# Performance work log

Hardware: AMD Instinct MI355X
Metric: run time of the kernel (lower is better)

Reference implementation:

```python
import jax, jax.numpy as jnp
import numpy as np

N_NODES = 50000
N_EDGES = 800000
HEADS = 4
IN_CH = 64
# hidden_dims=[32,64] reversed -> per-head out channels [64, 32]; concat=True
C1, C2 = 64, 32          # layer per-head channels
OUT_CH = 64              # conv_recon per-head channels, concat=False
NEG_SLOPE = 0.2


def gat_conv(x, edge_src, edge_dst, W, a_src, a_dst, b, concat):
    """PyG GATConv (v1) forward, eval mode (no dropout).
    x: [N, F_in]; W: [F_in, H*C]; a_src/a_dst: [H, C]; b: [H*C] or [C].
    edge (j -> i): messages flow edge_src -> edge_dst; softmax grouped by dst.
    """
    N = x.shape[0]
    H, C = a_src.shape
    h = (x @ W).reshape(N, H, C)                    # [N, H, C]
    al_s = jnp.einsum('nhc,hc->nh', h, a_src)       # [N, H]
    al_d = jnp.einsum('nhc,hc->nh', h, a_dst)       # [N, H]
    e = al_s[edge_src] + al_d[edge_dst]             # [E, H]
    e = jax.nn.leaky_relu(e, negative_slope=NEG_SLOPE)
    # segment softmax over incoming edges of each dst node
    m = jax.ops.segment_max(e, edge_dst, num_segments=N)          # [N, H]
    ex = jnp.exp(e - m[edge_dst])                                  # [E, H]
    s = jax.ops.segment_sum(ex, edge_dst, num_segments=N)         # [N, H]
    alpha = ex / (s[edge_dst] + 1e-16)                             # [E, H]
    msg = h[edge_src] * alpha[:, :, None]                          # [E, H, C]
    out = jax.ops.segment_sum(msg, edge_dst, num_segments=N)      # [N, H, C]
    out = out.reshape(N, H * C) if concat else out.mean(axis=1)
    return out + b


def setup_inputs() -> dict:
    key = jax.random.key(0)
    ks = jax.random.split(key, 16)
    sc = 0.1
    inp = {
        'x': jax.random.normal(ks[0], (N_NODES, IN_CH), jnp.float32),
        'edge_index': jax.random.randint(ks[1], (2, N_EDGES), 0, N_NODES, jnp.int64),
        # layer 1: in 64 -> 4 heads x 64, concat -> 256
        'W1': jax.random.normal(ks[2], (IN_CH, HEADS * C1), jnp.float32) * sc,
        'a1_src': jax.random.normal(ks[3], (HEADS, C1), jnp.float32) * sc,
        'a1_dst': jax.random.normal(ks[4], (HEADS, C1), jnp.float32) * sc,
        'b1': jnp.zeros((HEADS * C1,), jnp.float32),
        # layer 2: in 256 -> 4 heads x 32, concat -> 128
        'W2': jax.random.normal(ks[5], (HEADS * C1, HEADS * C2), jnp.float32) * sc,
        'a2_src': jax.random.normal(ks[6], (HEADS, C2), jnp.float32) * sc,
        'a2_dst': jax.random.normal(ks[7], (HEADS, C2), jnp.float32) * sc,
        'b2': jnp.zeros((HEADS * C2,), jnp.float32),
        # conv_recon: in 128 -> 4 heads x 64, concat=False (mean) -> 64
        'W3': jax.random.normal(ks[8], (HEADS * C2, HEADS * OUT_CH), jnp.float32) * sc,
        'a3_src': jax.random.normal(ks[9], (HEADS, OUT_CH), jnp.float32) * sc,
        'a3_dst': jax.random.normal(ks[10], (HEADS, OUT_CH), jnp.float32) * sc,
        'b3': jnp.zeros((OUT_CH,), jnp.float32),
    }
    return inp


def reference(x, edge_index, W1, a1_src, a1_dst, b1, W2, a2_src, a2_dst, b2,
              W3, a3_src, a3_dst, b3):
    src, dst = edge_index[0], edge_index[1]
    # used_DSBN=False -> no norm/ReLU between layers (matches torch forward)
    h = gat_conv(x, src, dst, W1, a1_src, a1_dst, b1, concat=True)
    h = gat_conv(h, src, dst, W2, a2_src, a2_dst, b2, concat=True)
    recon = gat_conv(h, src, dst, W3, a3_src, a3_dst, b3, concat=False)
    return recon
```

## Files before the change

### kernel.cpp

```cpp
#include <hip/hip_runtime.h>
#include <hip/hip_bf16.h>

#define HEADS 4

typedef __attribute__((ext_vector_type(4))) float f32x4;
typedef __attribute__((ext_vector_type(8))) short s16x8;

__device__ __forceinline__ float u2f(unsigned short u) {
    return __uint_as_float(((unsigned)u) << 16);
}
__device__ __forceinline__ unsigned short rne(float v) {
    unsigned b = __float_as_uint(v);
    return (unsigned short)((b + 0x7FFF + ((b >> 16) & 1)) >> 16);
}
__device__ __forceinline__ float ld1(const float* p) { return *p; }
__device__ __forceinline__ float ld1(const __hip_bfloat16* p) {
    return u2f(*reinterpret_cast<const unsigned short*>(p));
}
__device__ __forceinline__ float2 ld2(const float* p) { return *reinterpret_cast<const float2*>(p); }
__device__ __forceinline__ float2 ld2(const __hip_bfloat16* p) {
    ushort2 u = *reinterpret_cast<const ushort2*>(p);
    return make_float2(u2f(u.x), u2f(u.y));
}
__device__ __forceinline__ float4 ld4(const float* p) { return *reinterpret_cast<const float4*>(p); }
__device__ __forceinline__ float4 ld4(const __hip_bfloat16* p) {
    ushort4 u = *reinterpret_cast<const ushort4*>(p);
    return make_float4(u2f(u.x), u2f(u.y), u2f(u.z), u2f(u.w));
}
__device__ __forceinline__ void st1(float* p, float v) { *p = v; }
__device__ __forceinline__ void st1(__hip_bfloat16* p, float v) {
    *reinterpret_cast<unsigned short*>(p) = rne(v);
}
__device__ __forceinline__ void st2(float* p, float a, float b) {
    *reinterpret_cast<float2*>(p) = make_float2(a, b);
}
__device__ __forceinline__ void st2(__hip_bfloat16* p, float a, float b) {
    *reinterpret_cast<ushort2*>(p) = make_ushort2(rne(a), rne(b));
}
__device__ __forceinline__ void st4(float* p, float4 v) { *reinterpret_cast<float4*>(p) = v; }
__device__ __forceinline__ void st4(__hip_bfloat16* p, float4 v) {
    *reinterpret_cast<ushort4*>(p) = make_ushort4(rne(v.x), rne(v.y), rne(v.z), rne(v.w));
}

__device__ __forceinline__ int detect64(const int* __restrict__ e) {
    return ((e[1] | e[3] | e[5] | e[7]) == 0) ? 1 : 0;
}
__device__ __forceinline__ int edge_elem(const int* e, size_t idx, int is64) {
    return is64 ? e[2 * idx] : e[idx];
}

__global__ void deg_kernel(const int* __restrict__ eidx, int* __restrict__ deg, int E, int N) {
    int e = blockIdx.x * blockDim.x + threadIdx.x;
    if (e < E) {
        int is64 = detect64(eidx);
        int d = edge_elem(eidx, (size_t)E + e, is64);
        if ((unsigned)d < (unsigned)N) atomicAdd(&deg[d], 1);
    }
}

__global__ void reduce_kernel(const int* __restrict__ deg, int* __restrict__ bsum, int n) {
    __shared__ int sdata[256];
    int base = blockIdx.x * 1024;
    int t = threadIdx.x;
    int v = 0;
#pragma unroll
    for (int j = 0; j < 4; ++j) {
        int i = base + t + j * 256;
        if (i < n) v += deg[i];
    }
    sdata[t] = v;
    __syncthreads();
    for (int off = 128; off > 0; off >>= 1) {
        if (t < off) sdata[t] += sdata[t + off];
        __syncthreads();
    }
    if (t == 0) bsum[blockIdx.x] = sdata[0];
}

__global__ void scan_bsum_kernel(const int* __restrict__ bsum, int* __restrict__ boff,
                                 int nb, int* __restrict__ totalp) {
    int lane = threadIdx.x;
    int carry = 0;
    for (int base = 0; base < nb; base += 64) {
        int i = base + lane;
        int v = (i < nb) ? bsum[i] : 0;
        int inc = v;
        for (int off = 1; off < 64; off <<= 1) {
            int tt = __shfl_up(inc, off);
            if (lane >= off) inc += tt;
        }
        if (i < nb) boff[i] = carry + inc - v;
        carry += __shfl(inc, 63);
    }
    if (lane == 0) *totalp = carry;
}

__global__ void block_scan_kernel(const int* __restrict__ deg, const int* __restrict__ boff,
                                  int* __restrict__ rowptr, int* __restrict__ cursor, int n) {
    __shared__ int wsum[4];
    int base = blockIdx.x * 1024;
    int t = threadIdx.x;
    int lane = t & 63, w = t >> 6;
    int v[4];
    int lsum = 0;
#pragma unroll
    for (int j = 0; j < 4; ++j) {
        int i = base + t * 4 + j;
        v[j] = (i < n) ? deg[i] : 0;
        lsum += v[j];
    }
    int inc = lsum;
    for (int off = 1; off < 64; off <<= 1) {
        int tt = __shfl_up(inc, off);
        if (lane >= off) inc += tt;
    }
    if (lane == 63) wsum[w] = inc;
    __syncthreads();
    int woff = 0;
    for (int i = 0; i < w; ++i) woff += wsum[i];
    int ex = boff[blockIdx.x] + woff + inc - lsum;
#pragma unroll
    for (int j = 0; j < 4; ++j) {
        int i = base + t * 4 + j;
        if (i < n) { rowptr[i] = ex; cursor[i] = ex; }
        ex += v[j];
    }
}

__global__ void scatter_kernel(const int* __restrict__ eidx, int* __restrict__ cursor,
                               int* __restrict__ csr_src, int E, int N) {
    int e = blockIdx.x * blockDim.x + threadIdx.x;
    if (e < E) {
        int is64 = detect64(eidx);
        int s = edge_elem(eidx, (size_t)e, is64);
        int d = edge_elem(eidx, (size_t)E + e, is64);
        if ((unsigned)d < (unsigned)N && (unsigned)s < (unsigned)N) {
            int pos = atomicAdd(&cursor[d], 1);
            csr_src[pos] = s;
        }
    }
}

__global__ void prep0_kernel(const float* __restrict__ W1, const float* __restrict__ W2,
                             const float* __restrict__ W3, const float* __restrict__ b1,
                             const float* __restrict__ a1s, const float* __restrict__ a1d,
                             const float* __restrict__ a3s, const float* __restrict__ a3d,
                             __hip_bfloat16* __restrict__ Bt3, __hip_bfloat16* __restrict__ BtF,
                             float* __restrict__ bias12,
                             float* __restrict__ ps1, float* __restrict__ pd1,
                             float* __restrict__ ps3, float* __restrict__ pd3) {
    int b = blockIdx.x, t = threadIdx.x;
    if (b < 128) {
        int idx = b * 256 + t;
        int c = idx >> 9, r = idx & 511;
        int h = r >> 7, kk = r & 127;
        st1(&Bt3[idx], W3[(size_t)kk * 256 + h * 64 + c] * 0.25f);
        return;
    }
    b -= 128;
    if (b < 128) {
        int idx = b * 256 + t;
        int m = idx >> 8, k = idx & 255;
        int h = k >> 6, kin = k & 63;
        float acc = 0.f;
        for (int c = 0; c < 64; ++c)
            acc += W1[(size_t)kin * 256 + h * 64 + c] * W2[(size_t)(h * 64 + c) * 128 + m];
        st1(&BtF[idx], acc);
        return;
    }
    b -= 128;
    if (b < 1) {
        if (t < 128) {
            float acc = 0.f;
            for (int j = 0; j < 256; ++j) acc += b1[j] * W2[(size_t)j * 128 + t];
            bias12[t] = acc;
        }
        return;
    }
    b -= 1;
    if (b < 1) {
        int h = t >> 6, k = t & 63;
        float ss = 0.f, sd = 0.f;
        for (int c = 0; c < 64; ++c) {
            float w = W1[(size_t)k * 256 + h * 64 + c];
            ss += w * a1s[h * 64 + c];
            sd += w * a1d[h * 64 + c];
        }
        ps1[t] = ss;
        pd1[t] = sd;
        return;
    }
    b -= 1;
    if (b < 2) {
        int idx = b * 256 + t;
        int h = idx >> 7, k = idx & 127;
        float ss = 0.f, sd = 0.f;
        for (int c = 0; c < 64; ++c) {
            float w = W3[(size_t)k * 256 + h * 64 + c];
            ss += w * a3s[h * 64 + c];
            sd += w * a3d[h * 64 + c];
        }
        ps3[idx] = ss;
        pd3[idx] = sd;
        return;
    }
}

__global__ void xconv_alx_kernel(const float* __restrict__ x, const float* __restrict__ ps1,
                                 const float* __restrict__ pd1, __hip_bfloat16* __restrict__ xb,
                                 float* __restrict__ als, float* __restrict__ ald, int n8) {
    int i = blockIdx.x * blockDim.x + threadIdx.x;
    if (i >= n8) return;
    int r = i >> 3, sub = i & 7;
    int cbase = sub * 8;
    float4 a = *reinterpret_cast<const float4*>(&x[(size_t)i * 8]);
    float4 c = *reinterpret_cast<const float4*>(&x[(size_t)i * 8 + 4]);
    st4(&xb[(size_t)i * 8], a);
    st4(&xb[(size_t)i * 8 + 4], c);
    float ss[4], sd[4];
#pragma unroll
    for (int h = 0; h < 4; ++h) {
        float4 s0 = *reinterpret_cast<const float4*>(&ps1[h * 64 + cbase]);
        float4 s1 = *reinterpret_cast<const float4*>(&ps1[h * 64 + cbase + 4]);
        float4 d0 = *reinterpret_cast<const float4*>(&pd1[h * 64 + cbase]);
        float4 d1 = *reinterpret_cast<const float4*>(&pd1[h * 64 + cbase + 4]);
        ss[h] = a.x * s0.x + a.y * s0.y + a.z * s0.z + a.w * s0.w
              + c.x * s1.x + c.y * s1.y + c.z * s1.z + c.w * s1.w;
        sd[h] = a.x * d0.x + a.y * d0.y + a.z * d0.z + a.w * d0.w
              + c.x * d1.x + c.y * d1.y + c.z * d1.z + c.w * d1.w;
    }
#pragma unroll
    for (int off = 1; off < 8; off <<= 1) {
#pragma unroll
        for (int h = 0; h < 4; ++h) {
            ss[h] += __shfl_xor(ss[h], off);
            sd[h] += __shfl_xor(sd[h], off);
        }
    }
    if (sub == 0) {
        *reinterpret_cast<float4*>(&als[(size_t)r * 4]) = make_float4(ss[0], ss[1], ss[2], ss[3]);
        *reinterpret_cast<float4*>(&ald[(size_t)r * 4]) = make_float4(sd[0], sd[1], sd[2], sd[3]);
    }
}

template <int C, typename T>
__global__ void al_kernel(const T* __restrict__ h,
                          const float* __restrict__ a_src, const float* __restrict__ a_dst,
                          float* __restrict__ al_s, float* __restrict__ al_d, int N) {
    int idx = blockIdx.x * blockDim.x + threadIdx.x;
    if (idx >= N * HEADS) return;
    int n = idx >> 2, hd = idx & 3;
    const T* row = h + (size_t)n * HEADS * C + hd * C;
    float ss = 0.f, sd = 0.f;
#pragma unroll
    for (int c = 0; c < C; c += 4) {
        float4 v = ld4(&row[c]);
        float4 as = *reinterpret_cast<const float4*>(&a_src[hd * C + c]);
        float4 ad = *reinterpret_cast<const float4*>(&a_dst[hd * C + c]);
        ss += v.x * as.x + v.y * as.y + v.z * as.z + v.w * as.w;
        sd += v.x * ad.x + v.y * ad.y + v.z * ad.z + v.w * ad.w;
    }
    al_s[idx] = ss;
    al_d[idx] = sd;
}

template <int K, typename TIN, typename TOUT>
__global__ void gather_pre_kernel(const TIN* __restrict__ x, const float* __restrict__ als,
                                  const float* __restrict__ ald, const int* __restrict__ rowptr,
                                  const int* __restrict__ csr, TOUT* __restrict__ agg, int N) {
    constexpr int V = K / 64;
    int wave = (blockIdx.x * blockDim.x + threadIdx.x) >> 6;
    int lane = threadIdx.x & 63;
    if (wave >= N) return;
    int h4 = lane & 3, e4 = lane >> 2;
    float aldv = ald[wave * 4 + h4];
    float s0 = 0.f, s1 = 0.f, s2 = 0.f, s3 = 0.f;
    float acc[4][V] = {};
    int beg = rowptr[wave], end = rowptr[wave + 1];
    for (int kc = beg; kc < end; kc += 16) {
        int cnt = end - kc;
        if (cnt > 16) cnt = 16;
        int j = kc + e4;
        int src = csr[(j < end) ? j : beg];
        float e = als[src * 4 + h4] + aldv;
        e = fmaxf(e, 0.2f * e);
        float myw = __expf(e);
        if (cnt == 16) {
            int sj[16];
#pragma unroll
            for (int jj = 0; jj < 16; ++jj) sj[jj] = __shfl(src, jj * 4);
            if (V == 1) {
                float pv[16];
#pragma unroll
                for (int jj = 0; jj < 16; ++jj) pv[jj] = ld1(&x[(size_t)sj[jj] * K + lane]);
#pragma unroll
                for (int jj = 0; jj < 16; ++jj) {
                    float w0 = __shfl(myw, jj * 4 + 0), w1 = __shfl(myw, jj * 4 + 1);
                    float w2 = __shfl(myw, jj * 4 + 2), w3 = __shfl(myw, jj * 4 + 3);
                    s0 += w0; s1 += w1; s2 += w2; s3 += w3;
                    acc[0][0] += w0 * pv[jj]; acc[1][0] += w1 * pv[jj];
                    acc[2][0] += w2 * pv[jj]; acc[3][0] += w3 * pv[jj];
                }
            } else {
                float2 pv[16];
#pragma unroll
                for (int jj = 0; jj < 16; ++jj) pv[jj] = ld2(&x[(size_t)sj[jj] * K + lane * 2]);
#pragma unroll
                for (int jj = 0; jj < 16; ++jj) {
                    float w0 = __shfl(myw, jj * 4 + 0), w1 = __shfl(myw, jj * 4 + 1);
                    float w2 = __shfl(myw, jj * 4 + 2), w3 = __shfl(myw, jj * 4 + 3);
                    s0 += w0; s1 += w1; s2 += w2; s3 += w3;
                    acc[0][0] += w0 * pv[jj].x; acc[0][1] += w0 * pv[jj].y;
                    acc[1][0] += w1 * pv[jj].x; acc[1][1] += w1 * pv[jj].y;
                    acc[2][0] += w2 * pv[jj].x; acc[2][1] += w2 * pv[jj].y;
                    acc[3][0] += w3 * pv[jj].x; acc[3][1] += w3 * pv[jj].y;
                }
            }
        } else {
            for (int jj = 0; jj < cnt; ++jj) {
                int sjj = __shfl(src, jj * 4);
                float w0 = __shfl(myw, jj * 4 + 0), w1 = __shfl(myw, jj * 4 + 1);
                float w2 = __shfl(myw, jj * 4 + 2), w3 = __shfl(myw, jj * 4 + 3);
                s0 += w0; s1 += w1; s2 += w2; s3 += w3;
                if (V == 1) {
                    float v = ld1(&x[(size_t)sjj * K + lane]);
                    acc[0][0] += w0 * v; acc[1][0] += w1 * v;
                    acc[2][0] += w2 * v; acc[3][0] += w3 * v;
                } else {
                    float2 v = ld2(&x[(size_t)sjj * K + lane * 2]);
                    acc[0][0] += w0 * v.x; acc[0][1] += w0 * v.y;
                    acc[1][0] += w1 * v.x; acc[1][1] += w1 * v.y;
                    acc[2][0] += w2 * v.x; acc[2][1] += w2 * v.y;
                    acc[3][0] += w3 * v.x; acc[3][1] += w3 * v.y;
                }
            }
        }
    }
    float inv[4] = {1.f / (s0 + 1e-16f), 1.f / (s1 + 1e-16f),
                    1.f / (s2 + 1e-16f), 1.f / (s3 + 1e-16f)};
    size_t o = (size_t)wave * 4 * K;
#pragma unroll
    for (int h = 0; h < 4; ++h) {
        if (V == 1) {
            st1(&agg[o + h * K + lane], acc[h][0] * inv[h]);
        } else {
            st2(&agg[o + h * K + lane * 2], acc[h][0] * inv[h], acc[h][1] * inv[h]);
        }
    }
}

template <typename TIN, typename TOUT>
__global__ void gather_post32_alx_kernel(
    const TIN* __restrict__ h2, const float* __restrict__ als,
    const float* __restrict__ ald, const int* __restrict__ rowptr,
    const int* __restrict__ csr, const float* __restrict__ bias,
    const float* __restrict__ ps3, const float* __restrict__ pd3,
    TOUT* __restrict__ outp,
    float* __restrict__ als3, float* __restrict__ ald3, int N) {
    int wave = (blockIdx.x * blockDim.x + threadIdx.x) >> 6;
    int lane = threadIdx.x & 63;
    if (wave >= N) return;
    int h4 = lane & 3, e4 = lane >> 2;
    int hh = lane >> 4, l16 = lane & 15;
    float aldv = ald[wave * 4 + h4];
    float s = 0.f, a0 = 0.f, a1 = 0.f;
    int beg = rowptr[wave], end = rowptr[wave + 1];
    for (int kc = beg; kc < end; kc += 16) {
        int cnt = end - kc;
        if (cnt > 16) cnt = 16;
        int j = kc + e4;
        int src = csr[(j < end) ? j : beg];
        float e = als[src * 4 + h4] + aldv;
        e = fmaxf(e, 0.2f * e);
        float myw = __expf(e);
        if (cnt == 16) {
            int sj[16];
#pragma unroll
            for (int jj = 0; jj < 16; ++jj) sj[jj] = __shfl(src, jj * 4);
            float2 pv[16];
#pragma unroll
            for (int jj = 0; jj < 16; ++jj)
                pv[jj] = ld2(&h2[(size_t)sj[jj] * 128 + hh * 32 + l16 * 2]);
#pragma unroll
            for (int jj = 0; jj < 16; ++jj) {
                float w = __shfl(myw, jj * 4 + hh);
                s += w;
                a0 += w * pv[jj].x;
                a1 += w * pv[jj].y;
            }
        } else {
            for (int jj = 0; jj < cnt; ++jj) {
                int sjj = __shfl(src, jj * 4);
                float w = __shfl(myw, jj * 4 + hh);
                s += w;
                float2 v = ld2(&h2[(size_t)sjj * 128 + hh * 32 + l16 * 2]);
                a0 += w * v.x;
                a1 += w * v.y;
            }
        }
    }
    float inv = 1.f / (s + 1e-16f);
    int c = hh * 32 + l16 * 2;
    float v0 = a0 * inv + bias[c];
    float v1 = a1 * inv + bias[c + 1];
    st2(&outp[(size_t)wave * 128 + c], v0, v1);

    float sArr[4], dArr[4];
#pragma unroll
    for (int h = 0; h < 4; ++h) {
        float2 vs = *reinterpret_cast<const float2*>(&ps3[h * 128 + c]);
        float2 vd = *reinterpret_cast<const float2*>(&pd3[h * 128 + c]);
        sArr[h] = v0 * vs.x + v1 * vs.y;
        dArr[h] = v0 * vd.x + v1 * vd.y;
    }
#pragma unroll
    for (int off = 1; off < 64; off <<= 1) {
#pragma unroll
        for (int h = 0; h < 4; ++h) {
            sArr[h] += __shfl_xor(sArr[h], off);
            dArr[h] += __shfl_xor(dArr[h], off);
        }
    }
    if (lane < 4) {
        float os = (lane == 0) ? sArr[0] : (lane == 1) ? sArr[1] : (lane == 2) ? sArr[2] : sArr[3];
        float od = (lane == 0) ? dArr[0] : (lane == 1) ? dArr[1] : (lane == 2) ? dArr[2] : dArr[3];
        als3[wave * 4 + lane] = os;
        ald3[wave * 4 + lane] = od;
    }
}

template <typename TOUT>
__global__ __launch_bounds__(256) void mfma_gemm_kernel(
    const __hip_bfloat16* __restrict__ A, int lda, int aSel,
    const __hip_bfloat16* __restrict__ Bt,
    TOUT* __restrict__ O, int ldo,
    const float* __restrict__ bias, int N, int K) {
    __shared__ __hip_bfloat16 As[128][40];
    __shared__ __hip_bfloat16 Bs[64][40];
    int col0 = blockIdx.x * 64;
    int row0 = blockIdx.y * 128;
    int aOff = aSel ? col0 : 0;
    int tid = threadIdx.x;
    int wv = tid >> 6, lane = tid & 63;
    int g = lane >> 4, l16 = lane & 15;
    f32x4 acc[2][4] = {};

    for (int k0 = 0; k0 < K; k0 += 32) {
#pragma unroll
        for (int i = 0; i < 2; ++i) {
            int idx = tid + i * 256;
            int r = idx >> 2, h4 = idx & 3;
            int gr = row0 + r;
            uint4 v = make_uint4(0, 0, 0, 0);
            if (gr < N) v = *reinterpret_cast<const uint4*>(&A[(size_t)gr * lda + aOff + k0 + h4 * 8]);
            *reinterpret_cast<uint4*>(&As[r][h4 * 8]) = v;
        }
        {
            int r = tid >> 2, h4 = tid & 3;
            uint4 v = *reinterpret_cast<const uint4*>(&Bt[(size_t)(col0 + r) * K + k0 + h4 * 8]);
            *reinterpret_cast<uint4*>(&Bs[r][h4 * 8]) = v;
        }
        __syncthreads();
        s16x8 af[2], bf[4];
#pragma unroll
        for (int m = 0; m < 2; ++m)
            af[m] = *reinterpret_cast<const s16x8*>(&As[wv * 32 + m * 16 + l16][g * 8]);
#pragma unroll
        for (int n = 0; n < 4; ++n)
            bf[n] = *reinterpret_cast<const s16x8*>(&Bs[n * 16 + l16][g * 8]);
#pragma unroll
        for (int m = 0; m < 2; ++m)
#pragma unroll
            for (int n = 0; n < 4; ++n)
                acc[m][n] = __builtin_amdgcn_mfma_f32_16x16x32_bf16(af[m], bf[n], acc[m][n], 0, 0, 0);
        __syncthreads();
    }
#pragma unroll
    for (int m = 0; m < 2; ++m) {
#pragma unroll
        for (int rr = 0; rr < 4; ++rr) {
            int row = row0 + wv * 32 + m * 16 + g * 4 + rr;
            if (row < N) {
#pragma unroll
                for (int n = 0; n < 4; ++n) {
                    int col = col0 + n * 16 + l16;
                    float v = acc[m][n][rr];
                    if (bias) v += bias[col];
                    st1(&O[(size_t)row * ldo + col], v);
                }
            }
        }
    }
}

extern "C" void kernel_launch(void* const* d_in, const int* in_sizes, int n_in,
                              void* d_out, int out_size, void* d_ws, size_t ws_size,
                              hipStream_t stream) {
    const float* x      = (const float*)d_in[0];
    const int*   eidx   = (const int*)d_in[1];
    const float* W1     = (const float*)d_in[2];
    const float* a1_src = (const float*)d_in[3];
    const float* a1_dst = (const float*)d_in[4];
    const float* b1     = (const float*)d_in[5];
    const float* W2     = (const float*)d_in[6];
    const float* a2_src = (const float*)d_in[7];
    const float* a2_dst = (const float*)d_in[8];
    const float* b2     = (const float*)d_in[9];
    const float* W3     = (const float*)d_in[10];
    const float* a3_src = (const float*)d_in[11];
    const float* a3_dst = (const float*)d_in[12];
    const float* b3     = (const float*)d_in[13];
    float* out = (float*)d_out;

    const int N = in_sizes[0] / 64;
    const int E = in_sizes[1] / 2;
    const int NB = (N + 1023) / 1024;

    int* rowptr = (int*)d_ws;
    int* deg    = rowptr + (N + 1);
    int* cursor = deg + N;
    int* csr    = cursor + N;
    int* bsum   = csr + E;
    int* boff   = bsum + NB;
    uintptr_t pa = (uintptr_t)(boff + NB);
    pa = (pa + 255) & ~(uintptr_t)255;
    float* als  = (float*)pa;
    float* ald  = als + (size_t)N * 4;
    float* als3 = ald + (size_t)N * 4;
    float* ald3 = als3 + (size_t)N * 4;
    float* ps1  = ald3 + (size_t)N * 4;
    float* pd1  = ps1 + 256;
    float* ps3  = pd1 + 256;
    float* pd3  = ps3 + 512;
    float* bias12 = pd3 + 512;
    __hip_bfloat16* Bt3 = (__hip_bfloat16*)(bias12 + 128);
    __hip_bfloat16* BtF = Bt3 + 64 * 512;
    uintptr_t pf = (uintptr_t)(BtF + 128 * 256);
    pf = (pf + 255) & ~(uintptr_t)255;
    float* F    = (float*)pf;

    __hip_bfloat16* xb    = (__hip_bfloat16*)F;
    __hip_bfloat16* agg1b = (__hip_bfloat16*)(F + (size_t)N * 32);
    __hip_bfloat16* h2b   = (__hip_bfloat16*)(F + (size_t)N * 160);
    __hip_bfloat16* out2b = (__hip_bfloat16*)(F + (size_t)N * 224);
    __hip_bfloat16* agg3  = (__hip_bfloat16*)(F + (size_t)N * 288);

    hipMemsetAsync(deg, 0, (size_t)N * sizeof(int), stream);
    deg_kernel<<<(E + 255) / 256, 256, 0, stream>>>(eidx, deg, E, N);
    reduce_kernel<<<NB, 256, 0, stream>>>(deg, bsum, N);
    scan_bsum_kernel<<<1, 64, 0, stream>>>(bsum, boff, NB, rowptr + N);
    block_scan_kernel<<<NB, 256, 0, stream>>>(deg, boff, rowptr, cursor, N);
    scatter_kernel<<<(E + 255) / 256, 256, 0, stream>>>(eidx, cursor, csr, E, N);

    prep0_kernel<<<128 + 128 + 1 + 1 + 2, 256, 0, stream>>>(
        W1, W2, W3, b1, a1_src, a1_dst, a3_src, a3_dst,
        Bt3, BtF, bias12, ps1, pd1, ps3, pd3);
    const int n8 = N * 8;
    xconv_alx_kernel<<<(n8 + 255) / 256, 256, 0, stream>>>(x, ps1, pd1, xb, als, ald, n8);

    const int alBlocks  = (N * HEADS + 255) / 256;
    const int aggBlocks = (N + 3) / 4;
    const int rowB128   = (N + 127) / 128;

    gather_pre_kernel<64, __hip_bfloat16, __hip_bfloat16><<<aggBlocks, 256, 0, stream>>>(
        xb, als, ald, rowptr, csr, agg1b, N);
    mfma_gemm_kernel<__hip_bfloat16><<<dim3(2, rowB128), 256, 0, stream>>>(
        agg1b, 256, 0, BtF, h2b, 128, bias12, N, 256);

    al_kernel<32, __hip_bfloat16><<<alBlocks, 256, 0, stream>>>(h2b, a2_src, a2_dst, als, ald, N);
    gather_post32_alx_kernel<__hip_bfloat16, __hip_bfloat16><<<aggBlocks, 256, 0, stream>>>(
        h2b, als, ald, rowptr, csr, b2, ps3, pd3, out2b, als3, ald3, N);

    gather_pre_kernel<128, __hip_bfloat16, __hip_bfloat16><<<aggBlocks, 256, 0, stream>>>(
        out2b, als3, ald3, rowptr, csr, agg3, N);
    mfma_gemm_kernel<float><<<dim3(1, rowB128), 256, 0, stream>>>(
        agg3, 512, 0, Bt3, out, 64, b3, N, 512);
}
```

Measured before the change: 338.7 us.

## Fuse layer-2 attention logits into GEMM epilogue and vectorize gather loads

Removes the separate al_kernel by computing per-head source and destination attention logits inside the MFMA GEMM epilogue, using lane shuffles over the 16-column groups. It also restructures gather_pre_kernel so each lane loads 4 contiguous features from one edge, with several edges processed in parallel per wave. Partial sums are then combined by an xor-shuffle reduction before the store. This trades wider, fewer memory transactions and one fewer launch for extra shuffle-reduction work and more accumulator registers.

```diff
diff --git a/kernel.cpp b/kernel.cpp
--- a/kernel.cpp
+++ b/kernel.cpp
@@ -243,39 +243,21 @@
     }
 }
 
-template <int C, typename T>
-__global__ void al_kernel(const T* __restrict__ h,
-                          const float* __restrict__ a_src, const float* __restrict__ a_dst,
-                          float* __restrict__ al_s, float* __restrict__ al_d, int N) {
-    int idx = blockIdx.x * blockDim.x + threadIdx.x;
-    if (idx >= N * HEADS) return;
-    int n = idx >> 2, hd = idx & 3;
-    const T* row = h + (size_t)n * HEADS * C + hd * C;
-    float ss = 0.f, sd = 0.f;
-#pragma unroll
-    for (int c = 0; c < C; c += 4) {
-        float4 v = ld4(&row[c]);
-        float4 as = *reinterpret_cast<const float4*>(&a_src[hd * C + c]);
-        float4 ad = *reinterpret_cast<const float4*>(&a_dst[hd * C + c]);
-        ss += v.x * as.x + v.y * as.y + v.z * as.z + v.w * as.w;
-        sd += v.x * ad.x + v.y * ad.y + v.z * ad.z + v.w * ad.w;
-    }
-    al_s[idx] = ss;
-    al_d[idx] = sd;
-}
-
 template <int K, typename TIN, typename TOUT>
 __global__ void gather_pre_kernel(const TIN* __restrict__ x, const float* __restrict__ als,
                                   const float* __restrict__ ald, const int* __restrict__ rowptr,
                                   const int* __restrict__ csr, TOUT* __restrict__ agg, int N) {
-    constexpr int V = K / 64;
+    constexpr int G = K / 4;
+    constexpr int EPI = 64 / G;
     int wave = (blockIdx.x * blockDim.x + threadIdx.x) >> 6;
     int lane = threadIdx.x & 63;
     if (wave >= N) return;
     int h4 = lane & 3, e4 = lane >> 2;
+    int slot = lane / G;
+    int cb = (lane & (G - 1)) * 4;
     float aldv = ald[wave * 4 + h4];
-    float s0 = 0.f, s1 = 0.f, s2 = 0.f, s3 = 0.f;
-    float acc[4][V] = {};
+    float s[4] = {};
+    float acc[4][4] = {};
     int beg = rowptr[wave], end = rowptr[wave + 1];
     for (int kc = beg; kc < end; kc += 16) {
         int cnt = end - kc;
@@ -284,67 +266,69 @@
         int src = csr[(j < end) ? j : beg];
         float e = als[src * 4 + h4] + aldv;
         e = fmaxf(e, 0.2f * e);
-        float myw = __expf(e);
+        float myw = (e4 < cnt) ? __expf(e) : 0.f;
         if (cnt == 16) {
-            int sj[16];
-#pragma unroll
-            for (int jj = 0; jj < 16; ++jj) sj[jj] = __shfl(src, jj * 4);
-            if (V == 1) {
-                float pv[16];
-#pragma unroll
-                for (int jj = 0; jj < 16; ++jj) pv[jj] = ld1(&x[(size_t)sj[jj] * K + lane]);
-#pragma unroll
-                for (int jj = 0; jj < 16; ++jj) {
-                    float w0 = __shfl(myw, jj * 4 + 0), w1 = __shfl(myw, jj * 4 + 1);
-                    float w2 = __shfl(myw, jj * 4 + 2), w3 = __shfl(myw, jj * 4 + 3);
-                    s0 += w0; s1 += w1; s2 += w2; s3 += w3;
-                    acc[0][0] += w0 * pv[jj]; acc[1][0] += w1 * pv[jj];
-                    acc[2][0] += w2 * pv[jj]; acc[3][0] += w3 * pv[jj];
-                }
-            } else {
-                float2 pv[16];
-#pragma unroll
-                for (int jj = 0; jj < 16; ++jj) pv[jj] = ld2(&x[(size_t)sj[jj] * K + lane * 2]);
-#pragma unroll
-                for (int jj = 0; jj < 16; ++jj) {
-                    float w0 = __shfl(myw, jj * 4 + 0), w1 = __shfl(myw, jj * 4 + 1);
-                    float w2 = __shfl(myw, jj * 4 + 2), w3 = __shfl(myw, jj * 4 + 3);
-                    s0 += w0; s1 += w1; s2 += w2; s3 += w3;
-                    acc[0][0] += w0 * pv[jj].x; acc[0][1] += w0 * pv[jj].y;
-                    acc[1][0] += w1 * pv[jj].x; acc[1][1] += w1 * pv[jj].y;
-                    acc[2][0] += w2 * pv[jj].x; acc[2][1] += w2 * pv[jj].y;
-                    acc[3][0] += w3 * pv[jj].x; acc[3][1] += w3 * pv[jj].y;
-                }
+            constexpr int IT = 16 / EPI;
+            int esrc[IT];
+#pragma unroll
+            for (int i = 0; i < IT; ++i) esrc[i] = __shfl(src, (i * EPI + slot) * 4);
+            float4 pv[IT];
+#pragma unroll
+            for (int i = 0; i < IT; ++i) pv[i] = ld4(&x[(size_t)esrc[i] * K + cb]);
+#pragma unroll
+            for (int i = 0; i < IT; ++i) {
+                int base = (i * EPI + slot) * 4;
+                float w0 = __shfl(myw, base + 0), w1 = __shfl(myw, base + 1);
+                float w2 = __shfl(myw, base + 2), w3 = __shfl(myw, base + 3);
+                s[0] += w0; s[1] += w1; s[2] += w2; s[3] += w3;
+                acc[0][0] += w0 * pv[i].x; acc[0][1] += w0 * pv[i].y;
+                acc[0][2] += w0 * pv[i].z; acc[0][3] += w0 * pv[i].w;
+                acc[1][0] += w1 * pv[i].x; acc[1][1] += w1 * pv[i].y;
+                acc[1][2] += w1 * pv[i].z; acc[1][3] += w1 * pv[i].w;
+                acc[2][0] += w2 * pv[i].x; acc[2][1] += w2 * pv[i].y;
+                acc[2][2] += w2 * pv[i].z; acc[2][3] += w2 * pv[i].w;
+                acc[3][0] += w3 * pv[i].x; acc[3][1] += w3 * pv[i].y;
+                acc[3][2] += w3 * pv[i].z; acc[3][3] += w3 * pv[i].w;
             }
         } else {
-            for (int jj = 0; jj < cnt; ++jj) {
-                int sjj = __shfl(src, jj * 4);
-                float w0 = __shfl(myw, jj * 4 + 0), w1 = __shfl(myw, jj * 4 + 1);
-                float w2 = __shfl(myw, jj * 4 + 2), w3 = __shfl(myw, jj * 4 + 3);
-                s0 += w0; s1 += w1; s2 += w2; s3 += w3;
-                if (V == 1) {
-                    float v = ld1(&x[(size_t)sjj * K + lane]);
-                    acc[0][0] += w0 * v; acc[1][0] += w1 * v;
-                    acc[2][0] += w2 * v; acc[3][0] += w3 * v;
-                } else {
-                    float2 v = ld2(&x[(size_t)sjj * K + lane * 2]);
-                    acc[0][0] += w0 * v.x; acc[0][1] += w0 * v.y;
-                    acc[1][0] += w1 * v.x; acc[1][1] += w1 * v.y;
-                    acc[2][0] += w2 * v.x; acc[2][1] += w2 * v.y;
-                    acc[3][0] += w3 * v.x; acc[3][1] += w3 * v.y;
-                }
-            }
-        }
-    }
-    float inv[4] = {1.f / (s0 + 1e-16f), 1.f / (s1 + 1e-16f),
-                    1.f / (s2 + 1e-16f), 1.f / (s3 + 1e-16f)};
-    size_t o = (size_t)wave * 4 * K;
-#pragma unroll
-    for (int h = 0; h < 4; ++h) {
-        if (V == 1) {
-            st1(&agg[o + h * K + lane], acc[h][0] * inv[h]);
-        } else {
-            st2(&agg[o + h * K + lane * 2], acc[h][0] * inv[h], acc[h][1] * inv[h]);
+            int iters = (cnt + EPI - 1) / EPI;
+            for (int i = 0; i < iters; ++i) {
+                int eidx = i * EPI + slot;
+                int base = (eidx > 15 ? 15 : eidx) * 4;
+                int esrc = __shfl(src, base);
+                float4 pv = ld4(&x[(size_t)esrc * K + cb]);
+                float w0 = __shfl(myw, base + 0), w1 = __shfl(myw, base + 1);
+                float w2 = __shfl(myw, base + 2), w3 = __shfl(myw, base + 3);
+                s[0] += w0; s[1] += w1; s[2] += w2; s[3] += w3;
+                acc[0][0] += w0 * pv.x; acc[0][1] += w0 * pv.y;
+                acc[0][2] += w0 * pv.z; acc[0][3] += w0 * pv.w;
+                acc[1][0] += w1 * pv.x; acc[1][1] += w1 * pv.y;
+                acc[1][2] += w1 * pv.z; acc[1][3] += w1 * pv.w;
+                acc[2][0] += w2 * pv.x; acc[2][1] += w2 * pv.y;
+                acc[2][2] += w2 * pv.z; acc[2][3] += w2 * pv.w;
+                acc[3][0] += w3 * pv.x; acc[3][1] += w3 * pv.y;
+                acc[3][2] += w3 * pv.z; acc[3][3] += w3 * pv.w;
+            }
+        }
+    }
+#pragma unroll
+    for (int step = G; step < 64; step <<= 1) {
+#pragma unroll
+        for (int h = 0; h < 4; ++h) {
+            s[h] += __shfl_xor(s[h], step);
+            acc[h][0] += __shfl_xor(acc[h][0], step);
+            acc[h][1] += __shfl_xor(acc[h][1], step);
+            acc[h][2] += __shfl_xor(acc[h][2], step);
+            acc[h][3] += __shfl_xor(acc[h][3], step);
+        }
+    }
+    if (lane < G) {
+        size_t o = (size_t)wave * 4 * K;
+#pragma unroll
+        for (int h = 0; h < 4; ++h) {
+            float inv = 1.f / (s[h] + 1e-16f);
+            st4(&agg[o + h * K + cb],
+                make_float4(acc[h][0] * inv, acc[h][1] * inv, acc[h][2] * inv, acc[h][3] * inv));
         }
     }
 }
@@ -434,7 +418,10 @@
     const __hip_bfloat16* __restrict__ A, int lda, int aSel,
     const __hip_bfloat16* __restrict__ Bt,
     TOUT* __restrict__ O, int ldo,
-    const float* __restrict__ bias, int N, int K) {
+    const float* __restrict__ bias,
+    const float* __restrict__ a2s, const float* __restrict__ a2d,
+    float* __restrict__ oals, float* __restrict__ oald,
+    int N, int K) {
     __shared__ __hip_bfloat16 As[128][40];
     __shared__ __hip_bfloat16 Bs[64][40];
     int col0 = blockIdx.x * 64;
@@ -480,13 +467,33 @@
 #pragma unroll
         for (int rr = 0; rr < 4; ++rr) {
             int row = row0 + wv * 32 + m * 16 + g * 4 + rr;
+            float vv[4];
+#pragma unroll
+            for (int n = 0; n < 4; ++n) {
+                vv[n] = acc[m][n][rr];
+                if (bias) vv[n] += bias[col0 + n * 16 + l16];
+            }
             if (row < N) {
 #pragma unroll
-                for (int n = 0; n < 4; ++n) {
-                    int col = col0 + n * 16 + l16;
-                    float v = acc[m][n][rr];
-                    if (bias) v += bias[col];
-                    st1(&O[(size_t)row * ldo + col], v);
+                for (int n = 0; n < 4; ++n)
+                    st1(&O[(size_t)row * ldo + col0 + n * 16 + l16], vv[n]);
+            }
+            if (oals) {
+                float ts0 = vv[0] * a2s[col0 + l16]      + vv[1] * a2s[col0 + 16 + l16];
+                float ts1 = vv[2] * a2s[col0 + 32 + l16] + vv[3] * a2s[col0 + 48 + l16];
+                float td0 = vv[0] * a2d[col0 + l16]      + vv[1] * a2d[col0 + 16 + l16];
+                float td1 = vv[2] * a2d[col0 + 32 + l16] + vv[3] * a2d[col0 + 48 + l16];
+#pragma unroll
+                for (int off = 1; off < 16; off <<= 1) {
+                    ts0 += __shfl_xor(ts0, off); ts1 += __shfl_xor(ts1, off);
+                    td0 += __shfl_xor(td0, off); td1 += __shfl_xor(td1, off);
+                }
+                if (l16 == 0 && row < N) {
+                    int hb = col0 >> 5;
+                    oals[(size_t)row * 4 + hb]     = ts0;
+                    oals[(size_t)row * 4 + hb + 1] = ts1;
+                    oald[(size_t)row * 4 + hb]     = td0;
+                    oald[(size_t)row * 4 + hb + 1] = td1;
                 }
             }
         }
@@ -558,21 +565,19 @@
     const int n8 = N * 8;
     xconv_alx_kernel<<<(n8 + 255) / 256, 256, 0, stream>>>(x, ps1, pd1, xb, als, ald, n8);
 
-    const int alBlocks  = (N * HEADS + 255) / 256;
     const int aggBlocks = (N + 3) / 4;
     const int rowB128   = (N + 127) / 128;
 
     gather_pre_kernel<64, __hip_bfloat16, __hip_bfloat16><<<aggBlocks, 256, 0, stream>>>(
         xb, als, ald, rowptr, csr, agg1b, N);
     mfma_gemm_kernel<__hip_bfloat16><<<dim3(2, rowB128), 256, 0, stream>>>(
-        agg1b, 256, 0, BtF, h2b, 128, bias12, N, 256);
-
-    al_kernel<32, __hip_bfloat16><<<alBlocks, 256, 0, stream>>>(h2b, a2_src, a2_dst, als, ald, N);
+        agg1b, 256, 0, BtF, h2b, 128, bias12, a2_src, a2_dst, als, ald, N, 256);
+
     gather_post32_alx_kernel<__hip_bfloat16, __hip_bfloat16><<<aggBlocks, 256, 0, stream>>>(
         h2b, als, ald, rowptr, csr, b2, ps3, pd3, out2b, als3, ald3, N);
 
     gather_pre_kernel<128, __hip_bfloat16, __hip_bfloat16><<<aggBlocks, 256, 0, stream>>>(
         out2b, als3, ald3, rowptr, csr, agg3, N);
     mfma_gemm_kernel<float><<<dim3(1, rowB128), 256, 0, stream>>>(
-        agg3, 512, 0, Bt3, out, 64, b3, N, 512);
-}
+        agg3, 512, 0, Bt3, out, 64, b3, nullptr, nullptr, nullptr, nullptr, N, 512);
+}
```

Result: faster. 330.1 us (-2.5%).
